# Optimization experiments

Measured on AMD Instinct MI355X. Metric: run time of the kernel, lower is better.

The kernel has to match this reference:

```python
import jax, jax.numpy as jnp
import numpy as np

N, D_IN, D_BLOCK, D_OUT, E, K = 65536, 128, 256, 128, 8, 2


def setup_inputs() -> dict:
    key = jax.random.key(0)
    ks = jax.random.split(key, 8)
    s_in = 1.0 / np.sqrt(D_IN)
    s_h = 1.0 / np.sqrt(D_BLOCK)
    return {
        "x": jax.random.normal(ks[0], (N, D_IN), jnp.float32),
        "Wg": jax.random.normal(ks[1], (D_IN, E), jnp.float32) * s_in,
        "W1": jax.random.normal(ks[2], (E, D_IN, D_BLOCK), jnp.float32) * s_in,
        "b1": jax.random.normal(ks[3], (E, D_BLOCK), jnp.float32) * 0.01,
        "W2": jax.random.normal(ks[4], (E, D_BLOCK, D_BLOCK), jnp.float32) * s_h,
        "b2": jax.random.normal(ks[5], (E, D_BLOCK), jnp.float32) * 0.01,
        "Wo": jax.random.normal(ks[6], (D_BLOCK, D_OUT), jnp.float32) * s_h,
        "bo": jax.random.normal(ks[7], (D_OUT,), jnp.float32) * 0.01,
    }


def reference(x, Wg, W1, b1, W2, b2, Wo, bo):
    # Router: linear gate -> top-k -> softmax over the k selected logits,
    # scattered back to a dense [N, E] combine-weight matrix (zeros elsewhere).
    logits = x @ Wg                                   # [N, E]
    topv, topi = jax.lax.top_k(logits, K)             # [N, K]
    w_topk = jax.nn.softmax(topv, axis=-1)            # [N, K]
    onehot = jax.nn.one_hot(topi, E, dtype=x.dtype)   # [N, K, E]
    weights = jnp.einsum("nk,nke->ne", w_topk, onehot)  # [N, E]

    # Expert MLPs (n_blocks=2, ReLU, dropout=0 at eval), computed for all
    # experts over all tokens; unselected experts have weight 0, so the
    # weighted combine reproduces the original masked gather/scatter math.
    h = jax.nn.relu(jnp.einsum("nd,edh->enh", x, W1) + b1[:, None, :])   # [E,N,H]
    h = jax.nn.relu(jnp.einsum("enh,ehg->eng", h, W2) + b2[:, None, :])  # [E,N,H]
    y = jnp.einsum("enh,ho->eno", h, Wo) + bo                             # [E,N,O]

    # Weighted scatter-add combine: outs[n] = sum_e weights[n,e] * y[e,n]
    return jnp.einsum("ne,eno->no", weights, y)
```

## Files before the change

### kernel.cpp

```cpp
#include <hip/hip_runtime.h>
#include <math.h>

typedef unsigned short ushort_t;
typedef __attribute__((ext_vector_type(8))) short bf16x8;
typedef __attribute__((ext_vector_type(4))) float f32x4;
typedef __attribute__((ext_vector_type(8))) unsigned short u16x8;
typedef __attribute__((ext_vector_type(2))) unsigned int u32x2;
typedef __attribute__((ext_vector_type(4))) unsigned int u32x4;

#define N_TOK 65536
#define DIN 128
#define HD 256
#define DOUT 128
#define NEXP 8
#define MT 64
#define MAX_TILES (N_TOK / MT)

__device__ __forceinline__ unsigned short f2bf(float f) {
    union { float f; unsigned int i; } v; v.f = f;
    unsigned int i = v.i;
    return (unsigned short)((i + 0x7FFFu + ((i >> 16) & 1u)) >> 16);
}

#define RT_BLOCK 1024
#define RT_TPB 256
#define RT_PASS 128

__global__ __launch_bounds__(RT_BLOCK)
void router_kernel(const float* __restrict__ x,
                   const float* __restrict__ Wg,
                   const float* __restrict__ W1,
                   const float* __restrict__ W2,
                   const float* __restrict__ Wo,
                   int* __restrict__ counts,
                   int* __restrict__ list_tok,
                   float* __restrict__ list_w,
                   ushort_t* __restrict__ wt1f,
                   ushort_t* __restrict__ wt2f,
                   ushort_t* __restrict__ wotf) {
    __shared__ float xs[RT_PASS * 132];
    __shared__ float wgsT[NEXP * 132];
    __shared__ int lcnt[NEXP];
    __shared__ int lbase[NEXP];
    int tid = threadIdx.x;
    if (tid < NEXP) lcnt[tid] = 0;
    if (tid < DIN * NEXP) {
        int ee = tid & 7, k = tid >> 3;
        wgsT[ee * 132 + k] = Wg[tid];
    }
    if (tid < 400) {
        int id = blockIdx.x * 400 + tid;
        const float* src; ushort_t* dst; int Nn, ksteps, c;
        if (id < 32768) {
            int ee = id >> 12; c = id & 4095;
            Nn = HD; ksteps = 4; src = W1 + (size_t)ee * DIN * HD; dst = wt1f + (size_t)id * 8;
        } else if (id < 98304) {
            int t = id - 32768; int ee = t >> 13; c = t & 8191;
            Nn = HD; ksteps = 8; src = W2 + (size_t)ee * HD * HD; dst = wt2f + (size_t)t * 8;
        } else {
            int t = id - 98304; c = t;
            Nn = DOUT; ksteps = 8; src = Wo; dst = wotf + (size_t)t * 8;
        }
        int L = c & 63; int kc = c >> 6;
        int kstep = kc % ksteps; int ntile = kc / ksteps;
        int qq = L >> 4, mm = L & 15;
        int n = ntile * 16 + mm; int k0 = kstep * 32 + qq * 8;
        u16x8 v;
#pragma unroll
        for (int j = 0; j < 8; j++) v[j] = f2bf(src[(size_t)(k0 + j) * Nn + n]);
        *(u16x8*)dst = v;
    }

    int e = tid & 7;
    int tl = tid >> 3;
    int re0[2], re1[2], rp0[2], rp1[2];
    float rw0[2], rw1[2];

#pragma unroll
    for (int p = 0; p < 2; p++) {
        __syncthreads();
        {
            int row = tid >> 3;
            int f4 = tid & 7;
            const float4* src = (const float4*)(x + (size_t)(blockIdx.x * RT_TPB + p * RT_PASS + row) * DIN);
            float4* drow = (float4*)(xs + row * 132);
#pragma unroll
            for (int j = 0; j < 4; j++)
                drow[f4 + 8 * j] = src[f4 + 8 * j];
        }
        __syncthreads();

        const float4* xr = (const float4*)(xs + tl * 132);
        const float4* wv4 = (const float4*)(wgsT + e * 132);
        float lg = 0.f;
#pragma unroll 8
        for (int kk = 0; kk < 32; kk++) {
            float4 xv = xr[kk];
            float4 wv = wv4[kk];
            lg += xv.x * wv.x;
            lg += xv.y * wv.y;
            lg += xv.z * wv.z;
            lg += xv.w * wv.w;
        }
        float v0 = lg; int e0 = e;
#pragma unroll
        for (int d = 1; d < 8; d <<= 1) {
            float ov = __shfl_xor(v0, d, 64);
            int oe = __shfl_xor(e0, d, 64);
            if (ov > v0 || (ov == v0 && oe < e0)) { v0 = ov; e0 = oe; }
        }
        float mv = (e == e0) ? -3.0e38f : lg;
        float v1 = mv; int e1 = e;
#pragma unroll
        for (int d = 1; d < 8; d <<= 1) {
            float ov = __shfl_xor(v1, d, 64);
            int oe = __shfl_xor(e1, d, 64);
            if (ov > v1 || (ov == v1 && oe < e1)) { v1 = ov; e1 = oe; }
        }
        float t = expf(v1 - v0);
        float inv = 1.0f / (1.0f + t);
        re0[p] = e0; re1[p] = e1;
        rw0[p] = inv; rw1[p] = t * inv;
        if (e == 0) {
            rp0[p] = atomicAdd(&lcnt[e0], 1);
            rp1[p] = atomicAdd(&lcnt[e1], 1);
        }
    }
    __syncthreads();
    if (tid < NEXP) lbase[tid] = atomicAdd(&counts[tid * 32], lcnt[tid]);
    __syncthreads();
    if (e == 0) {
#pragma unroll
        for (int p = 0; p < 2; p++) {
            int n = blockIdx.x * RT_TPB + p * RT_PASS + tl;
            int q0 = lbase[re0[p]] + rp0[p];
            list_tok[re0[p] * N_TOK + q0] = n;
            list_w[re0[p] * N_TOK + q0] = -rw0[p];
            int q1 = lbase[re1[p]] + rp1[p];
            list_tok[re1[p] * N_TOK + q1] = n;
            list_w[re1[p] * N_TOK + q1] = rw1[p];
        }
    }
}

__global__ __launch_bounds__(256, 3)
void expert_kernel(const float* __restrict__ x,
                   const int* __restrict__ counts,
                   const int* __restrict__ list_tok,
                   const float* __restrict__ list_w,
                   const ushort_t* __restrict__ wt1f,
                   const ushort_t* __restrict__ wt2f,
                   const ushort_t* __restrict__ wotf,
                   const float* __restrict__ b1,
                   const float* __restrict__ b2,
                   const float* __restrict__ bo,
                   float* __restrict__ y2,
                   float* __restrict__ out) {
    int e = blockIdx.x & 7;
    int tile = blockIdx.x >> 3;
    int cnt = counts[e * 32];
    int base = tile * MT;
    if (base >= cnt) return;
    int rows = cnt - base; if (rows > MT) rows = MT;

    __shared__ __align__(16) ushort_t bufA[8192];
    __shared__ __align__(16) ushort_t bufH[16384];
    __shared__ int toks_s[MT];
    __shared__ float wts_s[MT];

    int tid = threadIdx.x;
    int lane = tid & 63;
    int w = tid >> 6;
    int q = lane >> 4;
    int mcol = lane & 15;

    const bf16x8* W1A = (const bf16x8*)(wt1f + (size_t)e * 4096 * 8);
    const bf16x8* W2A = (const bf16x8*)(wt2f + (size_t)e * 8192 * 8);
    const bf16x8* WoB = (const bf16x8*)wotf;
    const bf16x8* Albs = (const bf16x8*)bufA;
    const bf16x8* Hlbs = (const bf16x8*)bufH;

    if (tid < MT) {
        int rr = tid < rows ? tid : rows - 1;
        toks_s[tid] = list_tok[(size_t)e * N_TOK + base + rr];
        wts_s[tid] = list_w[(size_t)e * N_TOK + base + rr];
    }

    bf16x8 a1r[2][4];
#pragma unroll
    for (int rtl = 0; rtl < 4; rtl++)
        a1r[0][rtl] = W1A[((w * 4 + rtl) * 4 + 0) * 64 + lane];

    for (int c = tid; c < 1024; c += 256) {
        int row = c >> 4;
        int kchunk = c & 15;
        int rr = row < rows ? row : rows - 1;
        int tok = list_tok[(size_t)e * N_TOK + base + rr];
        const float4* src = (const float4*)(x + (size_t)tok * DIN + kchunk * 8);
        float4 lo = src[0], hi = src[1];
        unsigned p0, p1, p2, p3;
        asm("v_cvt_pk_bf16_f32 %0, %1, %2" : "=v"(p0) : "v"(lo.x), "v"(lo.y));
        asm("v_cvt_pk_bf16_f32 %0, %1, %2" : "=v"(p1) : "v"(lo.z), "v"(lo.w));
        asm("v_cvt_pk_bf16_f32 %0, %1, %2" : "=v"(p2) : "v"(hi.x), "v"(hi.y));
        asm("v_cvt_pk_bf16_f32 %0, %1, %2" : "=v"(p3) : "v"(hi.z), "v"(hi.w));
        int dchunk = ((kchunk >> 2) * 4 + (row >> 4)) * 64 + (kchunk & 3) * 16 + (row & 15);
        u32x4 v; v.x = p0; v.y = p1; v.z = p2; v.w = p3;
        *(u32x4*)(&bufA[dchunk * 8]) = v;
    }
    __syncthreads();

    f32x4 acc[4][4];
#pragma unroll
    for (int rtl = 0; rtl < 4; rtl++)
#pragma unroll
        for (int ct = 0; ct < 4; ct++) acc[rtl][ct] = (f32x4){0.f, 0.f, 0.f, 0.f};
#pragma unroll
    for (int ks = 0; ks < 4; ks++) {
        const int cur = ks & 1, nxt = cur ^ 1;
        if (ks < 3) {
#pragma unroll
            for (int rtl = 0; rtl < 4; rtl++)
                a1r[nxt][rtl] = W1A[((w * 4 + rtl) * 4 + ks + 1) * 64 + lane];
        }
        bf16x8 bf_[4];
#pragma unroll
        for (int ct = 0; ct < 4; ct++) bf_[ct] = Albs[(ks * 4 + ct) * 64 + lane];
#pragma unroll
        for (int rtl = 0; rtl < 4; rtl++)
#pragma unroll
            for (int ct = 0; ct < 4; ct++)
                acc[rtl][ct] = __builtin_amdgcn_mfma_f32_16x16x32_bf16(a1r[cur][rtl], bf_[ct], acc[rtl][ct], 0, 0, 0);
    }
    bf16x8 a2r[2][4];
#pragma unroll
    for (int rtl = 0; rtl < 4; rtl++)
        a2r[0][rtl] = W2A[((w * 4 + rtl) * 8 + 0) * 64 + lane];

    float4 b1v[4];
#pragma unroll
    for (int rtl = 0; rtl < 4; rtl++)
        b1v[rtl] = *(const float4*)(b1 + e * HD + w * 64 + rtl * 16 + q * 4);

#pragma unroll
    for (int rtl = 0; rtl < 4; rtl++) {
        int ks2 = w * 2 + (rtl >> 1);
        int q2 = (rtl * 2 + (q >> 1)) & 3;
        int uoff = (ks2 * 4 * 64 + q2 * 16 + mcol) * 8 + (q & 1) * 4;
#pragma unroll
        for (int ct = 0; ct < 4; ct++) {
            float v0 = acc[rtl][ct][0] + b1v[rtl].x; v0 = v0 > 0.f ? v0 : 0.f;
            float v1 = acc[rtl][ct][1] + b1v[rtl].y; v1 = v1 > 0.f ? v1 : 0.f;
            float v2 = acc[rtl][ct][2] + b1v[rtl].z; v2 = v2 > 0.f ? v2 : 0.f;
            float v3 = acc[rtl][ct][3] + b1v[rtl].w; v3 = v3 > 0.f ? v3 : 0.f;
            unsigned d0, d1;
            asm("v_cvt_pk_bf16_f32 %0, %1, %2" : "=v"(d0) : "v"(v0), "v"(v1));
            asm("v_cvt_pk_bf16_f32 %0, %1, %2" : "=v"(d1) : "v"(v2), "v"(v3));
            u32x2 dd; dd.x = d0; dd.y = d1;
            *(u32x2*)(&bufH[uoff + ct * 512]) = dd;
        }
    }
    __syncthreads();

    f32x4 acc2[4][4];
#pragma unroll
    for (int rtl = 0; rtl < 4; rtl++)
#pragma unroll
        for (int ct = 0; ct < 4; ct++) acc2[rtl][ct] = (f32x4){0.f, 0.f, 0.f, 0.f};
#pragma unroll
    for (int ks = 0; ks < 8; ks++) {
        const int cur = ks & 1, nxt = cur ^ 1;
        if (ks < 7) {
#pragma unroll
            for (int rtl = 0; rtl < 4; rtl++)
                a2r[nxt][rtl] = W2A[((w * 4 + rtl) * 8 + ks + 1) * 64 + lane];
        }
        bf16x8 bf_[4];
#pragma unroll
        for (int ct = 0; ct < 4; ct++) bf_[ct] = Hlbs[(ks * 4 + ct) * 64 + lane];
#pragma unroll
        for (int rtl = 0; rtl < 4; rtl++)
#pragma unroll
            for (int ct = 0; ct < 4; ct++)
                acc2[rtl][ct] = __builtin_amdgcn_mfma_f32_16x16x32_bf16(a2r[cur][rtl], bf_[ct], acc2[rtl][ct], 0, 0, 0);
    }
    bf16x8 b3r[2][2];
#pragma unroll
    for (int nt = 0; nt < 2; nt++)
        b3r[0][nt] = WoB[((w * 2 + nt) * 8 + 0) * 64 + lane];

    float4 b2v[4];
#pragma unroll
    for (int rtl = 0; rtl < 4; rtl++)
        b2v[rtl] = *(const float4*)(b2 + e * HD + w * 64 + rtl * 16 + q * 4);

    __syncthreads();

#pragma unroll
    for (int rtl = 0; rtl < 4; rtl++) {
        int ks2 = w * 2 + (rtl >> 1);
        int q2 = (rtl * 2 + (q >> 1)) & 3;
        int uoff = (ks2 * 4 * 64 + q2 * 16 + mcol) * 8 + (q & 1) * 4;
#pragma unroll
        for (int ct = 0; ct < 4; ct++) {
            float v0 = acc2[rtl][ct][0] + b2v[rtl].x; v0 = v0 > 0.f ? v0 : 0.f;
            float v1 = acc2[rtl][ct][1] + b2v[rtl].y; v1 = v1 > 0.f ? v1 : 0.f;
            float v2 = acc2[rtl][ct][2] + b2v[rtl].z; v2 = v2 > 0.f ? v2 : 0.f;
            float v3 = acc2[rtl][ct][3] + b2v[rtl].w; v3 = v3 > 0.f ? v3 : 0.f;
            unsigned d0, d1;
            asm("v_cvt_pk_bf16_f32 %0, %1, %2" : "=v"(d0) : "v"(v0), "v"(v1));
            asm("v_cvt_pk_bf16_f32 %0, %1, %2" : "=v"(d1) : "v"(v2), "v"(v3));
            u32x2 dd; dd.x = d0; dd.y = d1;
            *(u32x2*)(&bufH[uoff + ct * 512]) = dd;
        }
    }
    __syncthreads();

    f32x4 acc3[4][2];
#pragma unroll
    for (int mt = 0; mt < 4; mt++)
#pragma unroll
        for (int nt = 0; nt < 2; nt++) acc3[mt][nt] = (f32x4){0.f, 0.f, 0.f, 0.f};
#pragma unroll
    for (int ks = 0; ks < 8; ks++) {
        const int cur = ks & 1, nxt = cur ^ 1;
        if (ks < 7) {
#pragma unroll
            for (int nt = 0; nt < 2; nt++)
                b3r[nxt][nt] = WoB[((w * 2 + nt) * 8 + ks + 1) * 64 + lane];
        }
        bf16x8 af_[4];
#pragma unroll
        for (int mt = 0; mt < 4; mt++) af_[mt] = Hlbs[(ks * 4 + mt) * 64 + lane];
#pragma unroll
        for (int nt = 0; nt < 2; nt++)
#pragma unroll
            for (int mt = 0; mt < 4; mt++)
                acc3[mt][nt] = __builtin_amdgcn_mfma_f32_16x16x32_bf16(af_[mt], b3r[cur][nt], acc3[mt][nt], 0, 0, 0);
    }
#pragma unroll
    for (int mt = 0; mt < 4; mt++) {
#pragma unroll
        for (int r = 0; r < 4; r++) {
            int row = mt * 16 + q * 4 + r;
            if (row < rows) {
                int tok = toks_s[row];
                float wraw = wts_s[row];
                float wgt = fabsf(wraw);
                bool carrier = wraw < 0.f;
                float* dst = (carrier ? out : y2) + (size_t)tok * DOUT;
#pragma unroll
                for (int nt = 0; nt < 2; nt++) {
                    int col = (w * 2 + nt) * 16 + mcol;
                    dst[col] = wgt * acc3[mt][nt][r] + (carrier ? bo[col] : 0.f);
                }
            }
        }
    }
}

__global__ __launch_bounds__(256)
void combine_kernel(const float* __restrict__ y2, float* __restrict__ out) {
    int gid = blockIdx.x * 256 + threadIdx.x;
#pragma unroll
    for (int i = 0; i < 4; i++) {
        int idx = gid + i * (2048 * 256);
        float4 a = ((float4*)out)[idx];
        float4 b = ((const float4*)y2)[idx];
        a.x += b.x; a.y += b.y; a.z += b.z; a.w += b.w;
        ((float4*)out)[idx] = a;
    }
}

extern "C" void kernel_launch(void* const* d_in, const int* in_sizes, int n_in,
                              void* d_out, int out_size, void* d_ws, size_t ws_size,
                              hipStream_t stream) {
    const float* x  = (const float*)d_in[0];
    const float* Wg = (const float*)d_in[1];
    const float* W1 = (const float*)d_in[2];
    const float* b1 = (const float*)d_in[3];
    const float* W2 = (const float*)d_in[4];
    const float* b2 = (const float*)d_in[5];
    const float* Wo = (const float*)d_in[6];
    const float* bo = (const float*)d_in[7];
    float* out = (float*)d_out;

    char* ws = (char*)d_ws;
    size_t off = 0;
    int* counts    = (int*)(ws + off);    off += 1024;
    int* list_tok  = (int*)(ws + off);    off += (size_t)NEXP * N_TOK * 4;
    float* list_w  = (float*)(ws + off);  off += (size_t)NEXP * N_TOK * 4;
    ushort_t* wt1f = (ushort_t*)(ws + off); off += (size_t)NEXP * DIN * HD * 2;
    ushort_t* wt2f = (ushort_t*)(ws + off); off += (size_t)NEXP * HD * HD * 2;
    ushort_t* wotf = (ushort_t*)(ws + off); off += (size_t)HD * DOUT * 2;
    float* y2      = (float*)(ws + off);  off += (size_t)N_TOK * DOUT * 4;

    (void)hipMemsetAsync(counts, 0, 1024, stream);
    router_kernel<<<N_TOK / RT_TPB, RT_BLOCK, 0, stream>>>(
        x, Wg, W1, W2, Wo, counts, list_tok, list_w, wt1f, wt2f, wotf);
    expert_kernel<<<NEXP * MAX_TILES, 256, 0, stream>>>(x, counts, list_tok, list_w,
                                                        wt1f, wt2f, wotf, b1, b2, bo, y2, out);
    combine_kernel<<<2048, 256, 0, stream>>>(y2, out);
}
```

Before: 178.5 us.

## Drop register double-buffering of weight fragments, raise occupancy, add MFMA priority

Removes the register double-buffered prefetch of the W1/W2/Wo fragments in all three GEMM stages and loads each k-step's fragments just before use. This frees registers, and the launch bounds go from 3 to 4 waves per SIMD. s_setprio raises wave priority around the MFMA bursts so the extra resident waves interleave compute with other waves' loads. The risk is that each wave now stalls on its own global weight loads, and this only pays off if the added occupancy hides that latency; spills could follow if 4 waves does not fit.

```diff
diff --git a/kernel.cpp b/kernel.cpp
--- a/kernel.cpp
+++ b/kernel.cpp
@@ -143,7 +143,7 @@
     }
 }
 
-__global__ __launch_bounds__(256, 3)
+__global__ __launch_bounds__(256, 4)
 void expert_kernel(const float* __restrict__ x,
                    const int* __restrict__ counts,
                    const int* __restrict__ list_tok,
@@ -186,11 +186,6 @@
         wts_s[tid] = list_w[(size_t)e * N_TOK + base + rr];
     }
 
-    bf16x8 a1r[2][4];
-#pragma unroll
-    for (int rtl = 0; rtl < 4; rtl++)
-        a1r[0][rtl] = W1A[((w * 4 + rtl) * 4 + 0) * 64 + lane];
-
     for (int c = tid; c < 1024; c += 256) {
         int row = c >> 4;
         int kchunk = c & 15;
@@ -216,25 +211,21 @@
         for (int ct = 0; ct < 4; ct++) acc[rtl][ct] = (f32x4){0.f, 0.f, 0.f, 0.f};
 #pragma unroll
     for (int ks = 0; ks < 4; ks++) {
-        const int cur = ks & 1, nxt = cur ^ 1;
-        if (ks < 3) {
-#pragma unroll
-            for (int rtl = 0; rtl < 4; rtl++)
-                a1r[nxt][rtl] = W1A[((w * 4 + rtl) * 4 + ks + 1) * 64 + lane];
-        }
+        bf16x8 ar[4];
+#pragma unroll
+        for (int rtl = 0; rtl < 4; rtl++)
+            ar[rtl] = W1A[((w * 4 + rtl) * 4 + ks) * 64 + lane];
         bf16x8 bf_[4];
 #pragma unroll
         for (int ct = 0; ct < 4; ct++) bf_[ct] = Albs[(ks * 4 + ct) * 64 + lane];
+        __builtin_amdgcn_s_setprio(1);
 #pragma unroll
         for (int rtl = 0; rtl < 4; rtl++)
 #pragma unroll
             for (int ct = 0; ct < 4; ct++)
-                acc[rtl][ct] = __builtin_amdgcn_mfma_f32_16x16x32_bf16(a1r[cur][rtl], bf_[ct], acc[rtl][ct], 0, 0, 0);
-    }
-    bf16x8 a2r[2][4];
-#pragma unroll
-    for (int rtl = 0; rtl < 4; rtl++)
-        a2r[0][rtl] = W2A[((w * 4 + rtl) * 8 + 0) * 64 + lane];
+                acc[rtl][ct] = __builtin_amdgcn_mfma_f32_16x16x32_bf16(ar[rtl], bf_[ct], acc[rtl][ct], 0, 0, 0);
+        __builtin_amdgcn_s_setprio(0);
+    }
 
     float4 b1v[4];
 #pragma unroll
@@ -268,25 +259,21 @@
         for (int ct = 0; ct < 4; ct++) acc2[rtl][ct] = (f32x4){0.f, 0.f, 0.f, 0.f};
 #pragma unroll
     for (int ks = 0; ks < 8; ks++) {
-        const int cur = ks & 1, nxt = cur ^ 1;
-        if (ks < 7) {
-#pragma unroll
-            for (int rtl = 0; rtl < 4; rtl++)
-                a2r[nxt][rtl] = W2A[((w * 4 + rtl) * 8 + ks + 1) * 64 + lane];
-        }
+        bf16x8 ar[4];
+#pragma unroll
+        for (int rtl = 0; rtl < 4; rtl++)
+            ar[rtl] = W2A[((w * 4 + rtl) * 8 + ks) * 64 + lane];
         bf16x8 bf_[4];
 #pragma unroll
         for (int ct = 0; ct < 4; ct++) bf_[ct] = Hlbs[(ks * 4 + ct) * 64 + lane];
+        __builtin_amdgcn_s_setprio(1);
 #pragma unroll
         for (int rtl = 0; rtl < 4; rtl++)
 #pragma unroll
             for (int ct = 0; ct < 4; ct++)
-                acc2[rtl][ct] = __builtin_amdgcn_mfma_f32_16x16x32_bf16(a2r[cur][rtl], bf_[ct], acc2[rtl][ct], 0, 0, 0);
-    }
-    bf16x8 b3r[2][2];
-#pragma unroll
-    for (int nt = 0; nt < 2; nt++)
-        b3r[0][nt] = WoB[((w * 2 + nt) * 8 + 0) * 64 + lane];
+                acc2[rtl][ct] = __builtin_amdgcn_mfma_f32_16x16x32_bf16(ar[rtl], bf_[ct], acc2[rtl][ct], 0, 0, 0);
+        __builtin_amdgcn_s_setprio(0);
+    }
 
     float4 b2v[4];
 #pragma unroll
@@ -322,20 +309,20 @@
         for (int nt = 0; nt < 2; nt++) acc3[mt][nt] = (f32x4){0.f, 0.f, 0.f, 0.f};
 #pragma unroll
     for (int ks = 0; ks < 8; ks++) {
-        const int cur = ks & 1, nxt = cur ^ 1;
-        if (ks < 7) {
-#pragma unroll
-            for (int nt = 0; nt < 2; nt++)
-                b3r[nxt][nt] = WoB[((w * 2 + nt) * 8 + ks + 1) * 64 + lane];
-        }
+        bf16x8 br[2];
+#pragma unroll
+        for (int nt = 0; nt < 2; nt++)
+            br[nt] = WoB[((w * 2 + nt) * 8 + ks) * 64 + lane];
         bf16x8 af_[4];
 #pragma unroll
         for (int mt = 0; mt < 4; mt++) af_[mt] = Hlbs[(ks * 4 + mt) * 64 + lane];
+        __builtin_amdgcn_s_setprio(1);
 #pragma unroll
         for (int nt = 0; nt < 2; nt++)
 #pragma unroll
             for (int mt = 0; mt < 4; mt++)
-                acc3[mt][nt] = __builtin_amdgcn_mfma_f32_16x16x32_bf16(af_[mt], b3r[cur][nt], acc3[mt][nt], 0, 0, 0);
+                acc3[mt][nt] = __builtin_amdgcn_mfma_f32_16x16x32_bf16(af_[mt], br[nt], acc3[mt][nt], 0, 0, 0);
+        __builtin_amdgcn_s_setprio(0);
     }
 #pragma unroll
     for (int mt = 0; mt < 4; mt++) {
```

After: 179.9 us. Within noise of the previous version (+0.8%).
